# Kernel tuning notes

Hardware: AMD Instinct MI355X
Metric: run time of the kernel (lower is better)

The kernel has to match this reference:

```python
import jax, jax.numpy as jnp
import numpy as np

SCALE = 1.0 / np.float32(64.0 ** 0.5)  # hardcoded in source, not sqrt(d)


def setup_inputs() -> dict:
    key = jax.random.key(0)
    k1, k2 = jax.random.split(key)
    B, S, D, O = 8, 2048, 768, 768
    x = jax.random.normal(k1, (B, S, D), dtype=jnp.float32)
    kernel = jax.random.normal(k2, (3, D, O), dtype=jnp.float32) * 0.02
    return {"x": x, "kernel": kernel}


def reference(x, kernel):
    # x: [B,S,D], kernel: [3,D,O]
    WQ = jnp.einsum('bsd,do->bso', x, kernel[0])
    WK = jnp.einsum('bsd,do->bso', x, kernel[1])
    WV = jnp.einsum('bsd,do->bso', x, kernel[2])
    QK = jnp.einsum('bqo,bko->bqk', WQ, WK) * SCALE  # [B,S,S]
    A = jax.nn.softmax(QK, axis=-1)
    return jnp.einsum('bqk,bko->bqo', A, WV)  # [B,S,O]
```

## Files before the change

### kernel.cpp

```cpp
#include <hip/hip_runtime.h>

typedef unsigned short u16;
typedef __attribute__((ext_vector_type(8))) short short8;
typedef __attribute__((ext_vector_type(4))) float f32x4;
typedef __attribute__((ext_vector_type(8))) unsigned short ushort8;
typedef __attribute__((ext_vector_type(4))) unsigned short ushort4v;

__device__ __forceinline__ u16 f2bf(float f) {
    unsigned int u = __float_as_uint(f);
    u += 0x7FFFu + ((u >> 16) & 1u);
    return (u16)(u >> 16);
}
__device__ __forceinline__ float bf2f(u16 h) {
    return __uint_as_float(((unsigned int)h) << 16);
}

__device__ __forceinline__ void gld_lds16(const void* g, void* l) {
    __builtin_amdgcn_global_load_lds(
        (const __attribute__((address_space(1))) unsigned int*)g,
        (__attribute__((address_space(3))) unsigned int*)l,
        16, 0, 0);
}

template <int MODE>
__global__ __launch_bounds__(256) void gemm_bt(
    const u16* __restrict__ A, const u16* __restrict__ B,
    void* __restrict__ O0, void* __restrict__ O1, void* __restrict__ O2,
    float alpha)
{
    constexpr int K   = (MODE == 2) ? 2048 : 768;
    constexpr int lda = (MODE == 2) ? 2048 : 768;
    constexpr int ldb = (MODE == 2) ? 2048 : 768;

    __shared__ u16 As[128 * 64];
    __shared__ u16 Bs[128 * 64];

    const int f = blockIdx.x;
    const int xcd = f & 7;
    const int u = f >> 3;

    int tm, bn, cn, which = 0;
    long aoff = 0, boff = 0;
    if constexpr (MODE == 0) {
        const int c = u >> 4;
        const int rl = u & 15;
        tm = (xcd * 16 + rl) * 128;
        bn = c * 128;
        which = c / 6;
        cn = (c % 6) * 128;
    } else if constexpr (MODE == 1) {
        const int p = u >> 6, t = u & 63, c = t >> 2, rl = t & 3;
        tm = (p * 4 + rl) * 128;
        bn = cn = c * 128;
        aoff = (long)xcd * 2048 * 768;
        boff = aoff;
    } else {
        const int p = u / 12, t = u % 12, c = t >> 1, rl = t & 1;
        tm = (p * 2 + rl) * 128;
        bn = cn = c * 128;
        aoff = (long)xcd * 2048 * 2048;
        boff = (long)xcd * 768 * 2048;
    }

    const u16* Ab = A + aoff;
    const u16* Bb = B + boff;

    const int tid  = threadIdx.x;
    const int lane = tid & 63;
    const int wave = tid >> 6;
    const int wr = wave >> 1;
    const int wc = wave & 1;

    f32x4 acc[4][4] = {};

    const int srow = tid >> 3;
    const int kc   = (tid & 7) ^ (srow & 7);
    const long a_off = (long)(tm + srow) * lda + kc * 8;
    const long b_off = (long)(bn + srow) * ldb + kc * 8;

    for (int k0 = 0; k0 < K; k0 += 64) {
        __syncthreads();
#pragma unroll
        for (int p = 0; p < 4; ++p) {
            gld_lds16(Ab + a_off + (long)p * 32 * lda + k0, (void*)(As + tid * 8 + p * 2048));
            gld_lds16(Bb + b_off + (long)p * 32 * ldb + k0, (void*)(Bs + tid * 8 + p * 2048));
        }
        __syncthreads();

#pragma unroll
        for (int h = 0; h < 2; ++h) {
            const int swz = ((((h << 2) | (lane >> 4)) ^ (lane & 7)) << 3);
            const u16* a_base = As + (wr * 64 + (lane & 15)) * 64 + swz;
            const u16* b_base = Bs + (wc * 64 + (lane & 15)) * 64 + swz;
            short8 a[4], b[4];
#pragma unroll
            for (int i = 0; i < 4; ++i) a[i] = *(const short8*)(a_base + i * 1024);
#pragma unroll
            for (int j = 0; j < 4; ++j) b[j] = *(const short8*)(b_base + j * 1024);
#pragma unroll
            for (int i = 0; i < 4; ++i)
#pragma unroll
                for (int j = 0; j < 4; ++j)
                    acc[i][j] = __builtin_amdgcn_mfma_f32_16x16x32_bf16(
                        a[i], b[j], acc[i][j], 0, 0, 0);
        }
    }

#pragma unroll
    for (int i = 0; i < 4; ++i) {
        const int row0 = tm + wr * 64 + i * 16 + ((lane >> 4) << 2);
#pragma unroll
        for (int j = 0; j < 4; ++j) {
            const int col = cn + wc * 64 + j * 16 + (lane & 15);
#pragma unroll
            for (int r = 0; r < 4; ++r) {
                const int row = row0 + r;
                const float val = acc[i][j][r] * alpha;
                if constexpr (MODE == 0) {
                    if (which == 0)
                        ((u16*)O0)[(long)row * 768 + col] = f2bf(val);
                    else if (which == 1)
                        ((u16*)O1)[(long)row * 768 + col] = f2bf(val);
                    else
                        ((u16*)O2)[((long)(row >> 11) * 768 + col) * 2048 + (row & 2047)] = f2bf(val);
                } else if constexpr (MODE == 1) {
                    ((u16*)O0)[(long)xcd * 2048 * 2048 + (long)row * 2048 + col] = f2bf(val);
                } else {
                    ((float*)O0)[(long)xcd * 2048 * 768 + (long)row * 768 + col] = val;
                }
            }
        }
    }
}

__global__ __launch_bounds__(256) void cvt_x_kernel(
    const float4* __restrict__ x, ushort4v* __restrict__ out, int n4)
{
    int i = blockIdx.x * 256 + threadIdx.x;
    if (i < n4) {
        float4 f = x[i];
        ushort4v o;
        o.x = f2bf(f.x); o.y = f2bf(f.y); o.z = f2bf(f.z); o.w = f2bf(f.w);
        out[i] = o;
    }
}

__global__ __launch_bounds__(256) void cvt_w_kernel(
    const float* __restrict__ w, u16* __restrict__ wt)
{
    int i = blockIdx.x * 256 + threadIdx.x;
    int d = i % 768;
    int o = (i / 768) % 768;
    int m = i / (768 * 768);
    wt[i] = f2bf(w[((long)m * 768 + d) * 768 + o]);
}

__global__ __launch_bounds__(256) void softmax_kernel(u16* __restrict__ S)
{
    const long row = blockIdx.x;
    u16* p = S + row * 2048;
    const int t = threadIdx.x;
    const int lane = t & 63;
    const int wave = t >> 6;
    __shared__ float red[8];

    ushort8 raw = *(const ushort8*)(p + t * 8);
    float v[8];
    float m = -1e30f;
#pragma unroll
    for (int i = 0; i < 8; ++i) { v[i] = bf2f(raw[i]); m = fmaxf(m, v[i]); }
#pragma unroll
    for (int off = 1; off < 64; off <<= 1) m = fmaxf(m, __shfl_xor(m, off, 64));
    if (lane == 0) red[wave] = m;
    __syncthreads();
    m = fmaxf(fmaxf(red[0], red[1]), fmaxf(red[2], red[3]));

    float s = 0.f;
#pragma unroll
    for (int i = 0; i < 8; ++i) { v[i] = __expf(v[i] - m); s += v[i]; }
#pragma unroll
    for (int off = 1; off < 64; off <<= 1) s += __shfl_xor(s, off, 64);
    if (lane == 0) red[4 + wave] = s;
    __syncthreads();
    s = (red[4] + red[5]) + (red[6] + red[7]);

    const float inv = 1.0f / s;
    ushort8 out;
#pragma unroll
    for (int i = 0; i < 8; ++i) out[i] = f2bf(v[i] * inv);
    *(ushort8*)(p + t * 8) = out;
}

extern "C" void kernel_launch(void* const* d_in, const int* in_sizes, int n_in,
                              void* d_out, int out_size, void* d_ws, size_t ws_size,
                              hipStream_t stream)
{
    const float* x  = (const float*)d_in[0];
    const float* wk = (const float*)d_in[1];
    float* out = (float*)d_out;

    char* ws = (char*)d_ws;
    u16* xbf = (u16*)(ws);
    u16* wt  = (u16*)(ws + 25165824);
    u16* qbf = (u16*)(ws + 28704768);
    u16* kbf = (u16*)(ws + 53870592);
    u16* vt  = (u16*)(ws + 79036416);
    u16* S   = (u16*)(ws + 104202240);

    cvt_x_kernel<<<dim3(12288), dim3(256), 0, stream>>>(
        (const float4*)x, (ushort4v*)xbf, 3145728);
    cvt_w_kernel<<<dim3(6912), dim3(256), 0, stream>>>(wk, wt);

    gemm_bt<0><<<dim3(2304), dim3(256), 0, stream>>>(
        xbf, wt, qbf, kbf, vt, 1.0f);

    gemm_bt<1><<<dim3(2048), dim3(256), 0, stream>>>(
        qbf, kbf, S, nullptr, nullptr, 0.125f);

    softmax_kernel<<<dim3(16384), dim3(256), 0, stream>>>(S);

    gemm_bt<2><<<dim3(768), dim3(256), 0, stream>>>(
        S, vt, out, nullptr, nullptr, 1.0f);
}
```

Before: 362.8 us.

## Load GEMM MFMA operands directly from global memory, dropping LDS staging

The GEMM kernel no longer stages A and B tiles in shared memory through global_load_lds with barriers. Each wave now loads its MFMA fragments straight from global memory into registers, with a K loop unrolled by 128, and launch bounds request 3 blocks per SU. This removes the LDS round trip and the __syncthreads calls. In exchange, tiles are no longer shared across waves, so global and L2 traffic roughly doubles and per-lane loads are 16-byte reads strided by row, which may coalesce poorly.

```diff
diff --git a/kernel.cpp b/kernel.cpp
--- a/kernel.cpp
+++ b/kernel.cpp
@@ -15,15 +15,8 @@
     return __uint_as_float(((unsigned int)h) << 16);
 }
 
-__device__ __forceinline__ void gld_lds16(const void* g, void* l) {
-    __builtin_amdgcn_global_load_lds(
-        (const __attribute__((address_space(1))) unsigned int*)g,
-        (__attribute__((address_space(3))) unsigned int*)l,
-        16, 0, 0);
-}
-
 template <int MODE>
-__global__ __launch_bounds__(256) void gemm_bt(
+__global__ __launch_bounds__(256, 3) void gemm_bt(
     const u16* __restrict__ A, const u16* __restrict__ B,
     void* __restrict__ O0, void* __restrict__ O1, void* __restrict__ O2,
     float alpha)
@@ -31,9 +24,6 @@
     constexpr int K   = (MODE == 2) ? 2048 : 768;
     constexpr int lda = (MODE == 2) ? 2048 : 768;
     constexpr int ldb = (MODE == 2) ? 2048 : 768;
-
-    __shared__ u16 As[128 * 64];
-    __shared__ u16 Bs[128 * 64];
 
     const int f = blockIdx.x;
     const int xcd = f & 7;
@@ -62,41 +52,33 @@
         boff = (long)xcd * 768 * 2048;
     }
 
-    const u16* Ab = A + aoff;
-    const u16* Bb = B + boff;
-
     const int tid  = threadIdx.x;
     const int lane = tid & 63;
     const int wave = tid >> 6;
     const int wr = wave >> 1;
     const int wc = wave & 1;
+    const int q  = lane >> 4;
+    const int r  = lane & 15;
+
+    const u16* ap[4];
+    const u16* bp[4];
+#pragma unroll
+    for (int i = 0; i < 4; ++i)
+        ap[i] = A + aoff + (long)(tm + wr * 64 + i * 16 + r) * lda + q * 8;
+#pragma unroll
+    for (int j = 0; j < 4; ++j)
+        bp[j] = B + boff + (long)(bn + wc * 64 + j * 16 + r) * ldb + q * 8;
 
     f32x4 acc[4][4] = {};
 
-    const int srow = tid >> 3;
-    const int kc   = (tid & 7) ^ (srow & 7);
-    const long a_off = (long)(tm + srow) * lda + kc * 8;
-    const long b_off = (long)(bn + srow) * ldb + kc * 8;
-
-    for (int k0 = 0; k0 < K; k0 += 64) {
-        __syncthreads();
-#pragma unroll
-        for (int p = 0; p < 4; ++p) {
-            gld_lds16(Ab + a_off + (long)p * 32 * lda + k0, (void*)(As + tid * 8 + p * 2048));
-            gld_lds16(Bb + b_off + (long)p * 32 * ldb + k0, (void*)(Bs + tid * 8 + p * 2048));
-        }
-        __syncthreads();
-
-#pragma unroll
-        for (int h = 0; h < 2; ++h) {
-            const int swz = ((((h << 2) | (lane >> 4)) ^ (lane & 7)) << 3);
-            const u16* a_base = As + (wr * 64 + (lane & 15)) * 64 + swz;
-            const u16* b_base = Bs + (wc * 64 + (lane & 15)) * 64 + swz;
+    for (int k0 = 0; k0 < K; k0 += 128) {
+#pragma unroll
+        for (int kk = 0; kk < 128; kk += 32) {
             short8 a[4], b[4];
 #pragma unroll
-            for (int i = 0; i < 4; ++i) a[i] = *(const short8*)(a_base + i * 1024);
-#pragma unroll
-            for (int j = 0; j < 4; ++j) b[j] = *(const short8*)(b_base + j * 1024);
+            for (int i = 0; i < 4; ++i) a[i] = *(const short8*)(ap[i] + k0 + kk);
+#pragma unroll
+            for (int j = 0; j < 4; ++j) b[j] = *(const short8*)(bp[j] + k0 + kk);
 #pragma unroll
             for (int i = 0; i < 4; ++i)
 #pragma unroll
@@ -113,9 +95,9 @@
         for (int j = 0; j < 4; ++j) {
             const int col = cn + wc * 64 + j * 16 + (lane & 15);
 #pragma unroll
-            for (int r = 0; r < 4; ++r) {
-                const int row = row0 + r;
-                const float val = acc[i][j][r] * alpha;
+            for (int rr = 0; rr < 4; ++rr) {
+                const int row = row0 + rr;
+                const float val = acc[i][j][rr] * alpha;
                 if constexpr (MODE == 0) {
                     if (which == 0)
                         ((u16*)O0)[(long)row * 768 + col] = f2bf(val);
```

After: 698.3 us. 92.5% more time.
